# Optimization experiments

Measured on AMD Instinct MI355X. Metric: run time of the kernel, lower is better.

The kernel has to match this reference:

```python
import jax, jax.numpy as jnp
import numpy as np

# Model dims (match init_kwargs)
D_MODEL = 512
N_LAYERS = 4
N_DIST = 32
N_CAT = 32
LATENT = N_DIST * N_CAT  # 1024
D_INNER = 2 * D_MODEL    # 1024 (mamba expand=2)
D_STATE = 16
DT_RANK = D_MODEL // 16  # 32
K = 4                    # depthwise conv kernel
BATCH, SEQ = 4, 1024


def setup_inputs() -> dict:
    key = jax.random.key(0)
    ks = jax.random.split(key, 12)
    f = lambda k, shape, s=0.02: (jax.random.normal(k, shape, jnp.float32) * s)
    inp = {
        "x": jax.random.normal(ks[0], (BATCH, SEQ, LATENT), jnp.float32),
        "lin1_w": f(ks[1], (LATENT, D_MODEL)),
        "lin1_b": jnp.zeros((D_MODEL,), jnp.float32),
        "norm_w": jnp.ones((N_LAYERS, D_MODEL), jnp.float32),
        "in_w": f(ks[2], (N_LAYERS, D_MODEL, 2 * D_INNER)),
        "conv_w": f(ks[3], (N_LAYERS, D_INNER, K), 0.1),
        "conv_b": jnp.zeros((N_LAYERS, D_INNER), jnp.float32),
        "xproj_w": f(ks[4], (N_LAYERS, D_INNER, DT_RANK + 2 * D_STATE)),
        "dt_w": f(ks[5], (N_LAYERS, DT_RANK, D_INNER)),
        "dt_b": f(ks[6], (N_LAYERS, D_INNER), 0.5),
        "A_log": jnp.log(jnp.broadcast_to(
            jnp.arange(1, D_STATE + 1, dtype=jnp.float32),
            (N_LAYERS, D_INNER, D_STATE))),
        "Dp": jnp.ones((N_LAYERS, D_INNER), jnp.float32),
        "out_w": f(ks[7], (N_LAYERS, D_INNER, D_MODEL)),
        "lin2_w": f(ks[8], (D_MODEL, LATENT)),
        "lin2_b": jnp.zeros((LATENT,), jnp.float32),
    }
    return inp


def _rmsnorm(x, w):
    return x * jax.lax.rsqrt(jnp.mean(x * x, axis=-1, keepdims=True) + 1e-5) * w


def _causal_dwconv(x, w, b):
    # x: (B,S,D), w: (D,K) -> depthwise causal conv1d, left-padded
    S = x.shape[1]
    xp = jnp.pad(x, ((0, 0), (K - 1, 0), (0, 0)))
    y = xp[:, 0:S, :] * w[:, 0]
    for k in range(1, K):
        y = y + xp[:, k:k + S, :] * w[:, k]
    return y + b


def _selective_scan(u, dt, Bm, Cm, A, Dvec):
    # u, dt: (B,S,D); Bm, Cm: (B,S,N); A: (D,N); Dvec: (D,)
    dA = jnp.exp(dt[..., None] * A)                               # (B,S,D,N)
    dBu = dt[..., None] * Bm[:, :, None, :] * u[..., None]        # (B,S,D,N)
    h0 = jnp.zeros((u.shape[0], u.shape[2], A.shape[1]), u.dtype)

    def step(h, inputs):
        dA_t, dBu_t, C_t = inputs
        h = dA_t * h + dBu_t                                       # (B,D,N)
        y = jnp.einsum('bdn,bn->bd', h, C_t)
        return h, y

    _, ys = jax.lax.scan(step, h0,
                         (dA.transpose(1, 0, 2, 3),
                          dBu.transpose(1, 0, 2, 3),
                          Cm.transpose(1, 0, 2)))
    return ys.transpose(1, 0, 2) + u * Dvec                       # (B,S,D)


def reference(x, lin1_w, lin1_b, norm_w, in_w, conv_w, conv_b, xproj_w,
              dt_w, dt_b, A_log, Dp, out_w, lin2_w, lin2_b):
    B, S, _ = x.shape
    h = x @ lin1_w + lin1_b                                       # (B,S,d_model)
    for l in range(N_LAYERS):
        resid = h
        hn = _rmsnorm(h, norm_w[l])
        xz = hn @ in_w[l]                                         # (B,S,2*d_inner)
        xp, z = jnp.split(xz, 2, axis=-1)
        xp = jax.nn.silu(_causal_dwconv(xp, conv_w[l], conv_b[l]))
        dbl = xp @ xproj_w[l]                                     # (B,S,dt_rank+2N)
        dt = jax.nn.softplus(dbl[..., :DT_RANK] @ dt_w[l] + dt_b[l])
        Bm = dbl[..., DT_RANK:DT_RANK + D_STATE]
        Cm = dbl[..., DT_RANK + D_STATE:]
        A = -jnp.exp(A_log[l])                                    # (d_inner, N)
        y = _selective_scan(xp, dt, Bm, Cm, A, Dp[l])
        y = y * jax.nn.silu(z)
        h = resid + y @ out_w[l]
    out = h @ lin2_w + lin2_b                                     # (B,S,latent)
    out = jax.nn.softmax(out.reshape(B, S, N_DIST, N_CAT), axis=-1)
    return out.reshape(B, S, N_DIST * N_CAT)
```

## Files before the change

kernel.cpp:

```cpp
#include <hip/hip_runtime.h>
#include <math.h>

#define D_MODEL 512
#define N_LAYERS 4
#define LATENT 1024
#define D_INNER 1024
#define D_STATE 16
#define DT_RANK 32
#define KCONV 4
#define BATCH 4
#define SEQ 1024
#define NTOK (BATCH * SEQ)
#define PCH 32
#define CLEN 32

typedef __attribute__((ext_vector_type(8))) short short8;
typedef __attribute__((ext_vector_type(4))) float floatx4;
typedef unsigned short ushort_t;

#define WC_VM4   0x0F74
#define WC_VM8   0x0F78
#define WC_VM0   0x0F70
#define WC_LGKM0 0xC07F

__device__ __forceinline__ ushort_t f2bf(float f) {
    union { float f; unsigned u; } v; v.f = f;
    unsigned r = v.u + 0x7FFFu + ((v.u >> 16) & 1u);
    return (ushort_t)(r >> 16);
}
__device__ __forceinline__ float bf2f(ushort_t u) {
    union { unsigned u; float f; } v; v.u = ((unsigned)u) << 16;
    return v.f;
}
__device__ __forceinline__ void gll16(const void* g, void* l) {
    __builtin_amdgcn_global_load_lds(
        (const __attribute__((address_space(1))) void*)g,
        (__attribute__((address_space(3))) void*)l, 16, 0, 0);
}

__global__ __launch_bounds__(512, 2) void gemm_bf16_t256(
    const ushort_t* __restrict__ A, int lda,
    const ushort_t* __restrict__ Bt, int ldb,
    ushort_t* __restrict__ Cb, int ldc,
    int M, int N, int K)
{
    __shared__ ushort_t As[2][16384];
    __shared__ ushort_t Bs[2][16384];

    const int gx = gridDim.x;
    const int nwg = gx * gridDim.y;
    const int orig = blockIdx.y * gx + blockIdx.x;
    const int qq = nwg >> 3, rr = nwg & 7;
    const int xcd = orig & 7, loc = orig >> 3;
    const int swz = (xcd < rr ? xcd * (qq + 1) : rr * (qq + 1) + (xcd - rr) * qq) + loc;
    const int m0 = (swz / gx) * 256;
    const int n0 = (swz % gx) * 256;

    const int tid = threadIdx.x;
    const int w = tid >> 6;
    const int lane = tid & 63;
    const int quad = lane >> 4;
    const int l16 = lane & 15;
    const int wm = (w & 1) * 128;
    const int wn = (w >> 1) * 64;

    const int srow = tid >> 3;
    const int schunk = ((tid & 7) ^ (srow & 7)) * 8;
    const ushort_t* ga = A + (size_t)(m0 + srow) * lda + schunk;
    const ushort_t* gb = Bt + (size_t)(n0 + srow) * ldb + schunk;
    const int lofs = tid * 8;

    const int swz0 = ((0 * 4 + quad) ^ (l16 & 7)) * 8;
    const int swz1 = ((1 * 4 + quad) ^ (l16 & 7)) * 8;

    floatx4 acc[8][4] = {};
    const int nt = K >> 6;

    #define STAGE(t, b)                                                         \
        do {                                                                    \
            const ushort_t* pa_ = ga + (t) * 64;                                \
            const ushort_t* pb_ = gb + (t) * 64;                                \
            _Pragma("unroll")                                                   \
            for (int q = 0; q < 4; q++) {                                       \
                gll16(pa_ + (size_t)(q * 64) * lda, &As[(b)][q * 4096 + lofs]); \
                gll16(pb_ + (size_t)(q * 64) * ldb, &Bs[(b)][q * 4096 + lofs]); \
            }                                                                   \
        } while (0)

    STAGE(0, 0);

    for (int kt = 0; kt < nt; kt++) {
        const int cur = kt & 1;
        if (kt + 1 < nt) {
            STAGE(kt + 1, 1 - cur);
            __builtin_amdgcn_s_waitcnt(WC_VM8);
        } else {
            __builtin_amdgcn_s_waitcnt(WC_VM0);
        }
        __builtin_amdgcn_s_barrier();

        {
            short8 af[8], bfr[4];
            #pragma unroll
            for (int i = 0; i < 8; i++)
                af[i] = *(const short8*)&As[cur][(wm + i * 16 + l16) * 64 + swz0];
            #pragma unroll
            for (int j = 0; j < 4; j++)
                bfr[j] = *(const short8*)&Bs[cur][(wn + j * 16 + l16) * 64 + swz0];
            __builtin_amdgcn_s_waitcnt(WC_LGKM0);
            #pragma unroll
            for (int i = 0; i < 8; i++)
                #pragma unroll
                for (int j = 0; j < 4; j++)
                    acc[i][j] = __builtin_amdgcn_mfma_f32_16x16x32_bf16(
                        af[i], bfr[j], acc[i][j], 0, 0, 0);
        }
        {
            short8 af[8], bfr[4];
            #pragma unroll
            for (int i = 0; i < 8; i++)
                af[i] = *(const short8*)&As[cur][(wm + i * 16 + l16) * 64 + swz1];
            #pragma unroll
            for (int j = 0; j < 4; j++)
                bfr[j] = *(const short8*)&Bs[cur][(wn + j * 16 + l16) * 64 + swz1];
            __builtin_amdgcn_s_waitcnt(WC_LGKM0);
            #pragma unroll
            for (int i = 0; i < 8; i++)
                #pragma unroll
                for (int j = 0; j < 4; j++)
                    acc[i][j] = __builtin_amdgcn_mfma_f32_16x16x32_bf16(
                        af[i], bfr[j], acc[i][j], 0, 0, 0);
        }
        __builtin_amdgcn_s_barrier();
    }
    #undef STAGE

    #pragma unroll
    for (int j = 0; j < 4; j++) {
        int n = n0 + wn + j * 16 + l16;
        #pragma unroll
        for (int i = 0; i < 8; i++) {
            int mrow = m0 + wm + i * 16 + quad * 4;
            #pragma unroll
            for (int rr2 = 0; rr2 < 4; rr2++)
                Cb[(size_t)(mrow + rr2) * ldc + n] = f2bf(acc[i][j][rr2]);
        }
    }
}

__global__ __launch_bounds__(256, 3) void gemm_bf16_tile(
    const ushort_t* __restrict__ A, int lda,
    const ushort_t* __restrict__ Bt, int ldb,
    float* __restrict__ C, ushort_t* __restrict__ Cb, int ldc,
    const float* __restrict__ bias,
    int M, int N, int K, int flags)
{
    __shared__ ushort_t As[3][4096];
    __shared__ ushort_t Bs[3][4096];

    const int gx = gridDim.x;
    const int nwg = gx * gridDim.y;
    const int orig = blockIdx.y * gx + blockIdx.x;
    const int qq = nwg >> 3, rr = nwg & 7;
    const int xcd = orig & 7, loc = orig >> 3;
    const int swz = (xcd < rr ? xcd * (qq + 1) : rr * (qq + 1) + (xcd - rr) * qq) + loc;
    const int m0 = (swz / gx) * 64;
    const int n0 = (swz % gx) * 64;

    const int tid = threadIdx.x;
    const int w = tid >> 6;
    const int lane = tid & 63;
    const int quad = lane >> 4;
    const int l16 = lane & 15;
    const int wm = (w & 1) * 32;
    const int wn = (w >> 1) * 32;

    const int srow = tid >> 3;
    const int schunk = ((tid & 7) ^ (srow & 7)) * 8;
    const ushort_t* ga = A + (size_t)(m0 + srow) * lda + schunk;
    const ushort_t* gb = Bt + (size_t)(n0 + srow) * ldb + schunk;
    const int lofs = tid * 8;

    const int swz0 = ((0 * 4 + quad) ^ (l16 & 7)) * 8;
    const int swz1 = ((1 * 4 + quad) ^ (l16 & 7)) * 8;

    floatx4 acc[2][2] = {};
    const int nt = K >> 6;

    #define STAGE(t, b)                                         \
        do {                                                    \
            const ushort_t* pa_ = ga + (t) * 64;                \
            const ushort_t* pb_ = gb + (t) * 64;                \
            gll16(pa_, &As[(b)][lofs]);                         \
            gll16(pa_ + (size_t)32 * lda, &As[(b)][2048 + lofs]); \
            gll16(pb_, &Bs[(b)][lofs]);                         \
            gll16(pb_ + (size_t)32 * ldb, &Bs[(b)][2048 + lofs]); \
        } while (0)

    STAGE(0, 0);
    if (nt > 1) STAGE(1, 1);

    int cur = 0;
    for (int kt = 0; kt < nt; kt++) {
        if (kt + 1 < nt) __builtin_amdgcn_s_waitcnt(WC_VM4);
        else             __builtin_amdgcn_s_waitcnt(WC_VM0);
        __builtin_amdgcn_s_barrier();
        __builtin_amdgcn_sched_barrier(0);

        if (kt + 2 < nt) {
            int nb = cur + 2; if (nb >= 3) nb -= 3;
            STAGE(kt + 2, nb);
        }

        short8 af[2][2], bfr[2][2];
        #pragma unroll
        for (int i = 0; i < 2; i++) {
            const int r = wm + i * 16 + l16;
            af[0][i] = *(const short8*)&As[cur][r * 64 + swz0];
            af[1][i] = *(const short8*)&As[cur][r * 64 + swz1];
        }
        #pragma unroll
        for (int j = 0; j < 2; j++) {
            const int r = wn + j * 16 + l16;
            bfr[0][j] = *(const short8*)&Bs[cur][r * 64 + swz0];
            bfr[1][j] = *(const short8*)&Bs[cur][r * 64 + swz1];
        }
        __builtin_amdgcn_s_waitcnt(WC_LGKM0);
        __builtin_amdgcn_sched_barrier(0);

        #pragma unroll
        for (int ks = 0; ks < 2; ks++)
            #pragma unroll
            for (int i = 0; i < 2; i++)
                #pragma unroll
                for (int j = 0; j < 2; j++)
                    acc[i][j] = __builtin_amdgcn_mfma_f32_16x16x32_bf16(
                        af[ks][i], bfr[ks][j], acc[i][j], 0, 0, 0);

        cur++; if (cur == 3) cur = 0;
    }
    #undef STAGE

    #pragma unroll
    for (int j = 0; j < 2; j++) {
        int n = n0 + wn + j * 16 + l16;
        float bv = (flags & 1) ? bias[n] : 0.f;
        bool do_sp = (flags & 4) && (n < 1024);
        float spb = do_sp ? bias[n] : 0.f;
        #pragma unroll
        for (int i = 0; i < 2; i++) {
            int mrow = m0 + wm + i * 16 + quad * 4;
            #pragma unroll
            for (int rr2 = 0; rr2 < 4; rr2++) {
                size_t idx = (size_t)(mrow + rr2) * ldc + n;
                float v = acc[i][j][rr2] + bv;
                if (do_sp) {
                    v += spb;
                    v = (v > 20.f) ? v : log1pf(__expf(v));
                }
                if (flags & 8) {
                    Cb[idx] = f2bf(v);
                } else {
                    if (flags & 2) v += C[idx];
                    C[idx] = v;
                    if (flags & 16) Cb[idx] = f2bf(v);
                }
            }
        }
    }
}

__global__ __launch_bounds__(256, 3) void gemm_stepA(
    const ushort_t* __restrict__ A,
    const ushort_t* __restrict__ Bt,
    float* __restrict__ Cpart)
{
    __shared__ ushort_t As[3][4096];
    __shared__ ushort_t Bs[3][4096];

    const int kq = blockIdx.x;
    const int m0 = blockIdx.y * 64;
    const int k0 = kq * 256;

    const int tid = threadIdx.x;
    const int w = tid >> 6;
    const int lane = tid & 63;
    const int quad = lane >> 4;
    const int l16 = lane & 15;
    const int wm = (w & 1) * 32;
    const int wn = (w >> 1) * 32;

    const int srow = tid >> 3;
    const int schunk = ((tid & 7) ^ (srow & 7)) * 8;
    const ushort_t* ga = A + (size_t)(m0 + srow) * 1024 + k0 + schunk;
    const ushort_t* gb = Bt + (size_t)srow * 1024 + k0 + schunk;
    const int lofs = tid * 8;

    const int swz0 = ((0 * 4 + quad) ^ (l16 & 7)) * 8;
    const int swz1 = ((1 * 4 + quad) ^ (l16 & 7)) * 8;

    floatx4 acc[2][2] = {};
    const int nt = 4;

    #define STAGE(t, b)                                            \
        do {                                                       \
            const ushort_t* pa_ = ga + (t) * 64;                   \
            const ushort_t* pb_ = gb + (t) * 64;                   \
            gll16(pa_, &As[(b)][lofs]);                            \
            gll16(pa_ + (size_t)32 * 1024, &As[(b)][2048 + lofs]); \
            gll16(pb_, &Bs[(b)][lofs]);                            \
            gll16(pb_ + (size_t)32 * 1024, &Bs[(b)][2048 + lofs]); \
        } while (0)

    STAGE(0, 0);
    STAGE(1, 1);

    int cur = 0;
    for (int kt = 0; kt < nt; kt++) {
        if (kt + 1 < nt) __builtin_amdgcn_s_waitcnt(WC_VM4);
        else             __builtin_amdgcn_s_waitcnt(WC_VM0);
        __builtin_amdgcn_s_barrier();
        __builtin_amdgcn_sched_barrier(0);

        if (kt + 2 < nt) {
            int nb = cur + 2; if (nb >= 3) nb -= 3;
            STAGE(kt + 2, nb);
        }

        short8 af[2][2], bfr[2][2];
        #pragma unroll
        for (int i = 0; i < 2; i++) {
            const int r = wm + i * 16 + l16;
            af[0][i] = *(const short8*)&As[cur][r * 64 + swz0];
            af[1][i] = *(const short8*)&As[cur][r * 64 + swz1];
        }
        #pragma unroll
        for (int j = 0; j < 2; j++) {
            const int r = wn + j * 16 + l16;
            bfr[0][j] = *(const short8*)&Bs[cur][r * 64 + swz0];
            bfr[1][j] = *(const short8*)&Bs[cur][r * 64 + swz1];
        }
        __builtin_amdgcn_s_waitcnt(WC_LGKM0);
        __builtin_amdgcn_sched_barrier(0);

        #pragma unroll
        for (int ks = 0; ks < 2; ks++)
            #pragma unroll
            for (int i = 0; i < 2; i++)
                #pragma unroll
                for (int j = 0; j < 2; j++)
                    acc[i][j] = __builtin_amdgcn_mfma_f32_16x16x32_bf16(
                        af[ks][i], bfr[ks][j], acc[i][j], 0, 0, 0);

        cur++; if (cur == 3) cur = 0;
    }
    #undef STAGE

    float* Cp = Cpart + (size_t)kq * NTOK * 64;
    #pragma unroll
    for (int j = 0; j < 2; j++) {
        int n = wn + j * 16 + l16;
        #pragma unroll
        for (int i = 0; i < 2; i++) {
            int mrow = m0 + wm + i * 16 + quad * 4;
            #pragma unroll
            for (int rr2 = 0; rr2 < 4; rr2++)
                Cp[(size_t)(mrow + rr2) * 64 + n] = acc[i][j][rr2];
        }
    }
}

__global__ __launch_bounds__(256) void reduce_dblr(
    const float* __restrict__ part, float* __restrict__ dblr,
    ushort_t* __restrict__ dblr_bf)
{
    const int i = blockIdx.x * 256 + threadIdx.x;
    const size_t st = (size_t)NTOK * 64;
    float s = part[i] + part[i + st] + part[i + 2 * st] + part[i + 3 * st];
    dblr[i] = s;
    dblr_bf[i] = f2bf(s);
}

__global__ __launch_bounds__(256) void build_w2t_kernel(
    const float* __restrict__ dt_w, ushort_t* __restrict__ w2t)
{
    const int idx = blockIdx.x * 256 + threadIdx.x;
    const int k = idx & 63;
    const int n = (idx >> 6) & 1023;
    const int l = idx >> 16;
    ushort_t v = 0;
    if (k < 32)
        v = f2bf(dt_w[((size_t)l * DT_RANK + k) * D_INNER + n]);
    w2t[((size_t)l * 1024 + n) * 64 + k] = v;
}

__global__ __launch_bounds__(256) void transpose_cast_b(
    const float* __restrict__ in0, ushort_t* __restrict__ out0, int K, int N,
    size_t in_ls, size_t out_ls)
{
    const float* in = in0 + (size_t)blockIdx.z * in_ls;
    ushort_t* out = out0 + (size_t)blockIdx.z * out_ls;
    __shared__ float tile[32][33];
    const int n0 = blockIdx.x * 32, k0 = blockIdx.y * 32;
    const int tx = threadIdx.x & 31, ty = threadIdx.x >> 5;
    #pragma unroll
    for (int i = 0; i < 4; i++)
        tile[ty + i * 8][tx] = in[(size_t)(k0 + ty + i * 8) * N + n0 + tx];
    __syncthreads();
    #pragma unroll
    for (int i = 0; i < 4; i++)
        out[(size_t)(n0 + ty + i * 8) * K + k0 + tx] = f2bf(tile[tx][ty + i * 8]);
}

__global__ __launch_bounds__(256) void cast_bf16_kernel(
    const float* __restrict__ in, ushort_t* __restrict__ out)
{
    const int i = blockIdx.x * 256 + threadIdx.x;
    out[i] = f2bf(in[i]);
}

__global__ __launch_bounds__(256) void rmsnorm_kernel(
    const float* __restrict__ x, const float* __restrict__ w,
    ushort_t* __restrict__ y)
{
    const int row = blockIdx.x;
    const float* xr = x + (size_t)row * D_MODEL;
    ushort_t* yr = y + (size_t)row * D_MODEL;
    const int tid = threadIdx.x;

    float v0 = xr[tid], v1 = xr[tid + 256];
    float ss = v0 * v0 + v1 * v1;
    #pragma unroll
    for (int off = 32; off > 0; off >>= 1) ss += __shfl_down(ss, off);

    __shared__ float wsum[4];
    __shared__ float scale_s;
    int wid = tid >> 6, lane = tid & 63;
    if (lane == 0) wsum[wid] = ss;
    __syncthreads();
    if (tid == 0) {
        float tot = wsum[0] + wsum[1] + wsum[2] + wsum[3];
        scale_s = 1.0f / sqrtf(tot / (float)D_MODEL + 1e-5f);
    }
    __syncthreads();
    float sc = scale_s;
    yr[tid] = f2bf(v0 * sc * w[tid]);
    yr[tid + 256] = f2bf(v1 * sc * w[tid + 256]);
}

__global__ __launch_bounds__(256) void conv_silu_kernel(
    const ushort_t* __restrict__ xz, const float* __restrict__ w,
    const float* __restrict__ bconv, ushort_t* __restrict__ outb)
{
    const int idx = blockIdx.x * 256 + threadIdx.x;
    const int d = idx & (D_INNER - 1);
    const int t = (idx >> 10) & (SEQ - 1);
    const int row = idx >> 10;
    const ushort_t* base = xz + (size_t)row * 2048 + d;

    float s = 0.f;
    #pragma unroll
    for (int k = 0; k < KCONV; k++) {
        int tt = t + k - (KCONV - 1);
        if (tt >= 0)
            s = fmaf(bf2f(base[(ptrdiff_t)(k - (KCONV - 1)) * 2048]), w[d * KCONV + k], s);
    }
    s += bconv[d];
    float r = s / (1.f + __expf(-s));
    outb[idx] = f2bf(r);
}

__global__ __launch_bounds__(256) void scan_pass1(
    const float* __restrict__ dtb, const float* __restrict__ bc,
    const ushort_t* __restrict__ ub, const float* __restrict__ A_log,
    float* __restrict__ hfin, float* __restrict__ sumdt)
{
    const int tid = threadIdx.x;
    const int b = blockIdx.x >> 7;
    const int p = (blockIdx.x >> 2) & 31;
    const int d = ((blockIdx.x & 3) << 8) + tid;
    const int t0 = p * CLEN;

    float A[D_STATE];
    #pragma unroll
    for (int n = 0; n < D_STATE; n++) A[n] = -expf(A_log[d * D_STATE + n]);

    float h[D_STATE] = {};
    float sdt = 0.f;

    const float* dtp = dtb + ((size_t)b * SEQ + t0) * 1024 + d;
    const float* bp  = bc + ((size_t)b * SEQ + t0) * 64 + 32;
    const ushort_t* up = ub + ((size_t)b * SEQ + t0) * D_INNER + d;

    for (int t = 0; t < CLEN; t++) {
        float dtv = dtp[(size_t)t * 1024];
        float uv  = bf2f(up[(size_t)t * D_INNER]);
        float dtu = dtv * uv;
        sdt += dtv;
        #pragma unroll
        for (int n = 0; n < D_STATE; n++)
            h[n] = fmaf(__expf(dtv * A[n]), h[n], dtu * bp[t * 64 + n]);
    }

    size_t base = (size_t)(b * PCH + p) * D_STATE * D_INNER + d;
    #pragma unroll
    for (int n = 0; n < D_STATE; n++) hfin[base + (size_t)n * D_INNER] = h[n];
    sumdt[(size_t)(b * PCH + p) * D_INNER + d] = sdt;
}

__global__ __launch_bounds__(256) void scan_pass2(
    const float* __restrict__ A_log, const float* __restrict__ sumdt,
    float* __restrict__ hc)
{
    const int tid = threadIdx.x;
    const int b = blockIdx.x >> 6;
    const int n = (blockIdx.x >> 2) & 15;
    const int d = ((blockIdx.x & 3) << 8) + tid;

    const float Aval = -expf(A_log[d * D_STATE + n]);

    float fin[PCH], sd[PCH];
    #pragma unroll
    for (int p = 0; p < PCH; p++) {
        fin[p] = hc[((size_t)(b * PCH + p) * D_STATE + n) * D_INNER + d];
        sd[p]  = sumdt[(size_t)(b * PCH + p) * D_INNER + d];
    }
    float h = 0.f;
    #pragma unroll
    for (int p = 0; p < PCH; p++) {
        hc[((size_t)(b * PCH + p) * D_STATE + n) * D_INNER + d] = h;
        h = fmaf(__expf(Aval * sd[p]), h, fin[p]);
    }
}

__global__ __launch_bounds__(256) void scan_pass3(
    const float* __restrict__ dtb, const float* __restrict__ bc,
    const ushort_t* __restrict__ xz, const float* __restrict__ A_log,
    const float* __restrict__ Dp, const float* __restrict__ hstart,
    ushort_t* ub)
{
    const int tid = threadIdx.x;
    const int b = blockIdx.x >> 7;
    const int p = (blockIdx.x >> 2) & 31;
    const int d = ((blockIdx.x & 3) << 8) + tid;
    const int t0 = p * CLEN;

    float A[D_STATE];
    #pragma unroll
    for (int n = 0; n < D_STATE; n++) A[n] = -expf(A_log[d * D_STATE + n]);
    const float Dv = Dp[d];

    float h[D_STATE];
    size_t base = (size_t)(b * PCH + p) * D_STATE * D_INNER + d;
    #pragma unroll
    for (int n = 0; n < D_STATE; n++) h[n] = hstart[base + (size_t)n * D_INNER];

    const float* dtp = dtb + ((size_t)b * SEQ + t0) * 1024 + d;
    const float* bp  = bc + ((size_t)b * SEQ + t0) * 64 + 32;
    const ushort_t* zp = xz + ((size_t)b * SEQ + t0) * 2048 + 1024 + d;
    ushort_t* up = ub + ((size_t)b * SEQ + t0) * D_INNER + d;

    for (int t = 0; t < CLEN; t++) {
        float dtv = dtp[(size_t)t * 1024];
        float uv  = bf2f(up[(size_t)t * D_INNER]);
        float zv  = bf2f(zp[(size_t)t * 2048]);
        float dtu = dtv * uv;
        float y = 0.f;
        #pragma unroll
        for (int n = 0; n < D_STATE; n++) {
            h[n] = fmaf(__expf(dtv * A[n]), h[n], dtu * bp[t * 64 + n]);
            y = fmaf(h[n], bp[t * 64 + 16 + n], y);
        }
        float res = fmaf(uv, Dv, y);
        res *= zv / (1.f + __expf(-zv));
        up[(size_t)t * D_INNER] = f2bf(res);
    }
}

__global__ __launch_bounds__(256) void softmax_kernel(
    const float* __restrict__ in, float* __restrict__ out)
{
    const int idx = blockIdx.x * 256 + threadIdx.x;
    float v = in[idx];
    float m = v;
    #pragma unroll
    for (int off = 16; off > 0; off >>= 1) m = fmaxf(m, __shfl_xor(m, off, 32));
    float e = expf(v - m);
    float s = e;
    #pragma unroll
    for (int off = 16; off > 0; off >>= 1) s += __shfl_xor(s, off, 32);
    out[idx] = e / s;
}

extern "C" void kernel_launch(void* const* d_in, const int* in_sizes, int n_in,
                              void* d_out, int out_size, void* d_ws, size_t ws_size,
                              hipStream_t stream)
{
    const float* x       = (const float*)d_in[0];
    const float* lin1_w  = (const float*)d_in[1];
    const float* lin1_b  = (const float*)d_in[2];
    const float* norm_w  = (const float*)d_in[3];
    const float* in_w    = (const float*)d_in[4];
    const float* conv_w  = (const float*)d_in[5];
    const float* conv_b  = (const float*)d_in[6];
    const float* xproj_w = (const float*)d_in[7];
    const float* dt_w    = (const float*)d_in[8];
    const float* dt_b    = (const float*)d_in[9];
    const float* A_log   = (const float*)d_in[10];
    const float* Dp      = (const float*)d_in[11];
    const float* out_w   = (const float*)d_in[12];
    const float* lin2_w  = (const float*)d_in[13];
    const float* lin2_b  = (const float*)d_in[14];
    float* outp = (float*)d_out;
    (void)ws_size; (void)in_sizes; (void)n_in; (void)out_size;

    float* ws = (float*)d_ws;
    const size_t F1M = 1u << 20;
    float* h     = ws;
    float* dtb   = h + 2 * F1M;
    float* dblr  = dtb + 4 * F1M;
    float* dpart = dblr + (size_t)NTOK * 64;
    float* sumdt = dpart + (size_t)4 * NTOK * 64;
    float* hfin  = sumdt + (size_t)BATCH * PCH * D_INNER;
    ushort_t* xzb     = (ushort_t*)(hfin + 2 * F1M);
    ushort_t* hn_bf   = xzb + 8 * F1M;
    ushort_t* xb      = hn_bf + 2 * F1M;
    ushort_t* dblr_bf = xb + 4 * F1M;
    ushort_t* lin1_wt = dblr_bf + (size_t)NTOK * 64;
    ushort_t* in_wt   = lin1_wt + (size_t)512 * 1024;
    ushort_t* out_wt  = in_wt + (size_t)4 * 2048 * 512;
    ushort_t* lin2_wt = out_wt + (size_t)4 * 512 * 1024;
    ushort_t* xw_t    = lin2_wt + (size_t)1024 * 512;
    ushort_t* w2t     = xw_t + (size_t)4 * 64 * 1024;

    dim3 blk(256);

    transpose_cast_b<<<dim3(512 / 32, 1024 / 32, 1), blk, 0, stream>>>(
        lin1_w, lin1_wt, LATENT, D_MODEL, 0, 0);
    transpose_cast_b<<<dim3(2048 / 32, 512 / 32, N_LAYERS), blk, 0, stream>>>(
        in_w, in_wt, 512, 2048, (size_t)512 * 2048, (size_t)2048 * 512);
    transpose_cast_b<<<dim3(512 / 32, 1024 / 32, N_LAYERS), blk, 0, stream>>>(
        out_w, out_wt, 1024, 512, (size_t)1024 * 512, (size_t)512 * 1024);
    transpose_cast_b<<<dim3(64 / 32, 1024 / 32, N_LAYERS), blk, 0, stream>>>(
        xproj_w, xw_t, 1024, 64, (size_t)1024 * 64, (size_t)64 * 1024);
    transpose_cast_b<<<dim3(1024 / 32, 512 / 32, 1), blk, 0, stream>>>(
        lin2_w, lin2_wt, D_MODEL, LATENT, 0, 0);
    build_w2t_kernel<<<dim3((N_LAYERS * 1024 * 64) / 256), blk, 0, stream>>>(
        dt_w, w2t);

    cast_bf16_kernel<<<dim3((NTOK * LATENT) / 256), blk, 0, stream>>>(x, xb);

    gemm_bf16_tile<<<dim3(D_MODEL / 64, NTOK / 64), blk, 0, stream>>>(
        xb, LATENT, lin1_wt, LATENT, h, nullptr, D_MODEL, lin1_b,
        NTOK, D_MODEL, LATENT, 1);

    for (int l = 0; l < N_LAYERS; l++) {
        const float* nw = norm_w + (size_t)l * D_MODEL;
        const float* cw = conv_w + (size_t)l * D_INNER * KCONV;
        const float* cb = conv_b + (size_t)l * D_INNER;
        const float* db = dt_b + (size_t)l * D_INNER;
        const float* al = A_log + (size_t)l * D_INNER * D_STATE;
        const float* dp = Dp + (size_t)l * D_INNER;
        const ushort_t* iwt = in_wt + (size_t)l * 2048 * 512;
        const ushort_t* owt = out_wt + (size_t)l * 512 * 1024;
        const ushort_t* xwt = xw_t + (size_t)l * 64 * 1024;
        const ushort_t* w2  = w2t + (size_t)l * 1024 * 64;

        rmsnorm_kernel<<<dim3(NTOK), blk, 0, stream>>>(h, nw, hn_bf);

        gemm_bf16_t256<<<dim3(2048 / 256, NTOK / 256), dim3(512), 0, stream>>>(
            hn_bf, D_MODEL, iwt, D_MODEL, xzb, 2048, NTOK, 2048, D_MODEL);

        conv_silu_kernel<<<dim3((NTOK * D_INNER) / 256), blk, 0, stream>>>(
            xzb, cw, cb, xb);

        gemm_stepA<<<dim3(4, NTOK / 64), blk, 0, stream>>>(xb, xwt, dpart);
        reduce_dblr<<<dim3((NTOK * 64) / 256), blk, 0, stream>>>(
            dpart, dblr, dblr_bf);

        gemm_bf16_tile<<<dim3(1024 / 64, NTOK / 64), blk, 0, stream>>>(
            dblr_bf, 64, w2, 64, dtb, nullptr, 1024, db,
            NTOK, 1024, 64, 4);

        scan_pass1<<<dim3(BATCH * PCH * (D_INNER / 256)), blk, 0, stream>>>(
            dtb, dblr, xb, al, hfin, sumdt);
        scan_pass2<<<dim3(BATCH * D_STATE * (D_INNER / 256)), blk, 0, stream>>>(
            al, sumdt, hfin);
        scan_pass3<<<dim3(BATCH * PCH * (D_INNER / 256)), blk, 0, stream>>>(
            dtb, dblr, xzb, al, dp, hfin, xb);

        gemm_bf16_tile<<<dim3(D_MODEL / 64, NTOK / 64), blk, 0, stream>>>(
            xb, D_INNER, owt, D_INNER, h, hn_bf, D_MODEL, nullptr,
            NTOK, D_MODEL, D_INNER, (l == N_LAYERS - 1) ? 18 : 2);
    }

    gemm_bf16_tile<<<dim3(LATENT / 64, NTOK / 64), blk, 0, stream>>>(
        hn_bf, D_MODEL, lin2_wt, D_MODEL, dtb, nullptr, LATENT, lin2_b,
        NTOK, LATENT, D_MODEL, 1);
    softmax_kernel<<<dim3((NTOK * LATENT) / 256), blk, 0, stream>>>(dtb, outp);
}
```

Baseline: 709.2 us.

## Fuse dt projection into scan passes and softmax into final GEMM epilogue

The dt = softplus(dblr[:32] @ dt_w + dt_b) GEMM is removed. Each scan pass now recomputes dt per timestep from shared-memory copies of the dblr chunk and the dt_w slice, held in registers, which avoids writing and reading the 4096x1024 fp32 dt tensor. The final lin2 GEMM applies the 32-wide categorical softmax in its epilogue using xor-shuffles within 16 lanes, which drops the separate softmax kernel and its intermediate buffer. The cost is 32 extra FMAs per timestep in both scan passes (the dt work is done twice), plus extra shared memory per block, which may lower occupancy.

```diff
diff --git a/kernel.cpp b/kernel.cpp
--- a/kernel.cpp
+++ b/kernel.cpp
@@ -241,6 +241,30 @@
     }
     #undef STAGE
 
+    if (flags & 32) {
+        #pragma unroll
+        for (int i = 0; i < 2; i++) {
+            #pragma unroll
+            for (int rr2 = 0; rr2 < 4; rr2++) {
+                float v0 = acc[i][0][rr2] + bias[n0 + wn + l16];
+                float v1 = acc[i][1][rr2] + bias[n0 + wn + 16 + l16];
+                float m = fmaxf(v0, v1);
+                #pragma unroll
+                for (int off = 1; off < 16; off <<= 1)
+                    m = fmaxf(m, __shfl_xor(m, off));
+                float e0 = __expf(v0 - m), e1 = __expf(v1 - m);
+                float s = e0 + e1;
+                #pragma unroll
+                for (int off = 1; off < 16; off <<= 1)
+                    s += __shfl_xor(s, off);
+                float inv = 1.f / s;
+                size_t row = (size_t)(m0 + wm + i * 16 + quad * 4 + rr2) * ldc;
+                C[row + n0 + wn + l16] = e0 * inv;
+                C[row + n0 + wn + 16 + l16] = e1 * inv;
+            }
+        }
+        return;
+    }
     #pragma unroll
     for (int j = 0; j < 2; j++) {
         int n = n0 + wn + j * 16 + l16;
@@ -371,27 +395,11 @@
 }
 
 __global__ __launch_bounds__(256) void reduce_dblr(
-    const float* __restrict__ part, float* __restrict__ dblr,
-    ushort_t* __restrict__ dblr_bf)
+    const float* __restrict__ part, float* __restrict__ dblr)
 {
     const int i = blockIdx.x * 256 + threadIdx.x;
     const size_t st = (size_t)NTOK * 64;
-    float s = part[i] + part[i + st] + part[i + 2 * st] + part[i + 3 * st];
-    dblr[i] = s;
-    dblr_bf[i] = f2bf(s);
-}
-
-__global__ __launch_bounds__(256) void build_w2t_kernel(
-    const float* __restrict__ dt_w, ushort_t* __restrict__ w2t)
-{
-    const int idx = blockIdx.x * 256 + threadIdx.x;
-    const int k = idx & 63;
-    const int n = (idx >> 6) & 1023;
-    const int l = idx >> 16;
-    ushort_t v = 0;
-    if (k < 32)
-        v = f2bf(dt_w[((size_t)l * DT_RANK + k) * D_INNER + n]);
-    w2t[((size_t)l * 1024 + n) * 64 + k] = v;
+    dblr[i] = part[i] + part[i + st] + part[i + 2 * st] + part[i + 3 * st];
 }
 
 __global__ __launch_bounds__(256) void transpose_cast_b(
@@ -471,15 +479,31 @@
 }
 
 __global__ __launch_bounds__(256) void scan_pass1(
-    const float* __restrict__ dtb, const float* __restrict__ bc,
-    const ushort_t* __restrict__ ub, const float* __restrict__ A_log,
+    const float* __restrict__ dblr, const ushort_t* __restrict__ ub,
+    const float* __restrict__ A_log, const float* __restrict__ dtw,
+    const float* __restrict__ dtbias,
     float* __restrict__ hfin, float* __restrict__ sumdt)
 {
     const int tid = threadIdx.x;
     const int b = blockIdx.x >> 7;
     const int p = (blockIdx.x >> 2) & 31;
-    const int d = ((blockIdx.x & 3) << 8) + tid;
+    const int d0 = (blockIdx.x & 3) << 8;
+    const int d = d0 + tid;
     const int t0 = p * CLEN;
+
+    __shared__ float w2s[32 * 256];
+    __shared__ float dbs[32 * 64];
+
+    for (int i = tid; i < 32 * 256; i += 256)
+        w2s[i] = dtw[(size_t)(i >> 8) * D_INNER + d0 + (i & 255)];
+    for (int i = tid; i < 32 * 64; i += 256)
+        dbs[i] = dblr[(size_t)(b * SEQ + t0 + (i >> 6)) * 64 + (i & 63)];
+    __syncthreads();
+
+    float w2c[32];
+    #pragma unroll
+    for (int k = 0; k < 32; k++) w2c[k] = w2s[k * 256 + tid];
+    const float bias_d = dtbias[d];
 
     float A[D_STATE];
     #pragma unroll
@@ -487,19 +511,20 @@
 
     float h[D_STATE] = {};
     float sdt = 0.f;
-
-    const float* dtp = dtb + ((size_t)b * SEQ + t0) * 1024 + d;
-    const float* bp  = bc + ((size_t)b * SEQ + t0) * 64 + 32;
     const ushort_t* up = ub + ((size_t)b * SEQ + t0) * D_INNER + d;
 
     for (int t = 0; t < CLEN; t++) {
-        float dtv = dtp[(size_t)t * 1024];
+        float accd = bias_d;
+        #pragma unroll
+        for (int k = 0; k < 32; k++)
+            accd = fmaf(dbs[t * 64 + k], w2c[k], accd);
+        float dtv = (accd > 20.f) ? accd : log1pf(__expf(accd));
         float uv  = bf2f(up[(size_t)t * D_INNER]);
         float dtu = dtv * uv;
         sdt += dtv;
         #pragma unroll
         for (int n = 0; n < D_STATE; n++)
-            h[n] = fmaf(__expf(dtv * A[n]), h[n], dtu * bp[t * 64 + n]);
+            h[n] = fmaf(__expf(dtv * A[n]), h[n], dtu * dbs[t * 64 + 32 + n]);
     }
 
     size_t base = (size_t)(b * PCH + p) * D_STATE * D_INNER + d;
@@ -534,16 +559,31 @@
 }
 
 __global__ __launch_bounds__(256) void scan_pass3(
-    const float* __restrict__ dtb, const float* __restrict__ bc,
-    const ushort_t* __restrict__ xz, const float* __restrict__ A_log,
-    const float* __restrict__ Dp, const float* __restrict__ hstart,
-    ushort_t* ub)
+    const float* __restrict__ dblr, const ushort_t* __restrict__ xz,
+    const float* __restrict__ A_log, const float* __restrict__ dtw,
+    const float* __restrict__ dtbias, const float* __restrict__ Dp,
+    const float* __restrict__ hstart, ushort_t* ub)
 {
     const int tid = threadIdx.x;
     const int b = blockIdx.x >> 7;
     const int p = (blockIdx.x >> 2) & 31;
-    const int d = ((blockIdx.x & 3) << 8) + tid;
+    const int d0 = (blockIdx.x & 3) << 8;
+    const int d = d0 + tid;
     const int t0 = p * CLEN;
+
+    __shared__ float w2s[32 * 256];
+    __shared__ float dbs[32 * 64];
+
+    for (int i = tid; i < 32 * 256; i += 256)
+        w2s[i] = dtw[(size_t)(i >> 8) * D_INNER + d0 + (i & 255)];
+    for (int i = tid; i < 32 * 64; i += 256)
+        dbs[i] = dblr[(size_t)(b * SEQ + t0 + (i >> 6)) * 64 + (i & 63)];
+    __syncthreads();
+
+    float w2c[32];
+    #pragma unroll
+    for (int k = 0; k < 32; k++) w2c[k] = w2s[k * 256 + tid];
+    const float bias_d = dtbias[d];
 
     float A[D_STATE];
     #pragma unroll
@@ -555,41 +595,28 @@
     #pragma unroll
     for (int n = 0; n < D_STATE; n++) h[n] = hstart[base + (size_t)n * D_INNER];
 
-    const float* dtp = dtb + ((size_t)b * SEQ + t0) * 1024 + d;
-    const float* bp  = bc + ((size_t)b * SEQ + t0) * 64 + 32;
     const ushort_t* zp = xz + ((size_t)b * SEQ + t0) * 2048 + 1024 + d;
     ushort_t* up = ub + ((size_t)b * SEQ + t0) * D_INNER + d;
 
     for (int t = 0; t < CLEN; t++) {
-        float dtv = dtp[(size_t)t * 1024];
+        float accd = bias_d;
+        #pragma unroll
+        for (int k = 0; k < 32; k++)
+            accd = fmaf(dbs[t * 64 + k], w2c[k], accd);
+        float dtv = (accd > 20.f) ? accd : log1pf(__expf(accd));
         float uv  = bf2f(up[(size_t)t * D_INNER]);
         float zv  = bf2f(zp[(size_t)t * 2048]);
         float dtu = dtv * uv;
         float y = 0.f;
         #pragma unroll
         for (int n = 0; n < D_STATE; n++) {
-            h[n] = fmaf(__expf(dtv * A[n]), h[n], dtu * bp[t * 64 + n]);
-            y = fmaf(h[n], bp[t * 64 + 16 + n], y);
+            h[n] = fmaf(__expf(dtv * A[n]), h[n], dtu * dbs[t * 64 + 32 + n]);
+            y = fmaf(h[n], dbs[t * 64 + 48 + n], y);
         }
         float res = fmaf(uv, Dv, y);
         res *= zv / (1.f + __expf(-zv));
         up[(size_t)t * D_INNER] = f2bf(res);
     }
-}
-
-__global__ __launch_bounds__(256) void softmax_kernel(
-    const float* __restrict__ in, float* __restrict__ out)
-{
-    const int idx = blockIdx.x * 256 + threadIdx.x;
-    float v = in[idx];
-    float m = v;
-    #pragma unroll
-    for (int off = 16; off > 0; off >>= 1) m = fmaxf(m, __shfl_xor(m, off, 32));
-    float e = expf(v - m);
-    float s = e;
-    #pragma unroll
-    for (int off = 16; off > 0; off >>= 1) s += __shfl_xor(s, off, 32);
-    out[idx] = e / s;
 }
 
 extern "C" void kernel_launch(void* const* d_in, const int* in_sizes, int n_in,
@@ -631,7 +658,6 @@
     ushort_t* out_wt  = in_wt + (size_t)4 * 2048 * 512;
     ushort_t* lin2_wt = out_wt + (size_t)4 * 512 * 1024;
     ushort_t* xw_t    = lin2_wt + (size_t)1024 * 512;
-    ushort_t* w2t     = xw_t + (size_t)4 * 64 * 1024;
 
     dim3 blk(256);
 
@@ -645,8 +671,6 @@
         xproj_w, xw_t, 1024, 64, (size_t)1024 * 64, (size_t)64 * 1024);
     transpose_cast_b<<<dim3(1024 / 32, 512 / 32, 1), blk, 0, stream>>>(
         lin2_w, lin2_wt, D_MODEL, LATENT, 0, 0);
-    build_w2t_kernel<<<dim3((N_LAYERS * 1024 * 64) / 256), blk, 0, stream>>>(
-        dt_w, w2t);
 
     cast_bf16_kernel<<<dim3((NTOK * LATENT) / 256), blk, 0, stream>>>(x, xb);
 
@@ -661,10 +685,10 @@
         const float* db = dt_b + (size_t)l * D_INNER;
         const float* al = A_log + (size_t)l * D_INNER * D_STATE;
         const float* dp = Dp + (size_t)l * D_INNER;
+        const float* dw = dt_w + (size_t)l * DT_RANK * D_INNER;
         const ushort_t* iwt = in_wt + (size_t)l * 2048 * 512;
         const ushort_t* owt = out_wt + (size_t)l * 512 * 1024;
         const ushort_t* xwt = xw_t + (size_t)l * 64 * 1024;
-        const ushort_t* w2  = w2t + (size_t)l * 1024 * 64;
 
         rmsnorm_kernel<<<dim3(NTOK), blk, 0, stream>>>(h, nw, hn_bf);
 
@@ -675,19 +699,14 @@
             xzb, cw, cb, xb);
 
         gemm_stepA<<<dim3(4, NTOK / 64), blk, 0, stream>>>(xb, xwt, dpart);
-        reduce_dblr<<<dim3((NTOK * 64) / 256), blk, 0, stream>>>(
-            dpart, dblr, dblr_bf);
-
-        gemm_bf16_tile<<<dim3(1024 / 64, NTOK / 64), blk, 0, stream>>>(
-            dblr_bf, 64, w2, 64, dtb, nullptr, 1024, db,
-            NTOK, 1024, 64, 4);
+        reduce_dblr<<<dim3((NTOK * 64) / 256), blk, 0, stream>>>(dpart, dblr);
 
         scan_pass1<<<dim3(BATCH * PCH * (D_INNER / 256)), blk, 0, stream>>>(
-            dtb, dblr, xb, al, hfin, sumdt);
+            dblr, xb, al, dw, db, hfin, sumdt);
         scan_pass2<<<dim3(BATCH * D_STATE * (D_INNER / 256)), blk, 0, stream>>>(
             al, sumdt, hfin);
         scan_pass3<<<dim3(BATCH * PCH * (D_INNER / 256)), blk, 0, stream>>>(
-            dtb, dblr, xzb, al, dp, hfin, xb);
+            dblr, xzb, al, dw, db, dp, hfin, xb);
 
         gemm_bf16_tile<<<dim3(D_MODEL / 64, NTOK / 64), blk, 0, stream>>>(
             xb, D_INNER, owt, D_INNER, h, hn_bf, D_MODEL, nullptr,
@@ -695,7 +714,6 @@
     }
 
     gemm_bf16_tile<<<dim3(LATENT / 64, NTOK / 64), blk, 0, stream>>>(
-        hn_bf, D_MODEL, lin2_wt, D_MODEL, dtb, nullptr, LATENT, lin2_b,
-        NTOK, LATENT, D_MODEL, 1);
-    softmax_kernel<<<dim3((NTOK * LATENT) / 256), blk, 0, stream>>>(dtb, outp);
-}
+        hn_bf, D_MODEL, lin2_wt, D_MODEL, outp, nullptr, LATENT, lin2_b,
+        NTOK, LATENT, D_MODEL, 1 | 32);
+}
```

Measured after the change: 789.4 us. 11.3% more time.
